# Kernel tuning notes

Measured on AMD Instinct MI355X. Metric: run time of the kernel, lower is better.

## Reference

```python
import jax, jax.numpy as jnp
import numpy as np

N, QLEN, KLEN = 4, 2048, 2048
QDIM = KVDIM = 512
EMBED, HEADS = 1024, 16
HEAD_DIM = EMBED // HEADS


def setup_inputs() -> dict:
    key = jax.random.key(0)
    ks = jax.random.split(key, 7)
    return {
        "queries": jax.random.normal(ks[0], (N, QLEN, QDIM), dtype=jnp.float32),
        "keys": jax.random.normal(ks[1], (1, KLEN, KVDIM), dtype=jnp.float32),
        "values": jax.random.normal(ks[2], (1, KLEN, KVDIM), dtype=jnp.float32),
        "mask": jax.random.randint(ks[3], (N, 1, 1, KLEN), 0, 2, dtype=jnp.int32),
        "Wq": jax.random.normal(ks[4], (QDIM, EMBED), dtype=jnp.float32) * (QDIM ** -0.5),
        "Wk": jax.random.normal(ks[5], (KVDIM, EMBED), dtype=jnp.float32) * (KVDIM ** -0.5),
        "Wv": jax.random.normal(ks[6], (KVDIM, EMBED), dtype=jnp.float32) * (KVDIM ** -0.5),
    }


def reference(queries, keys, values, mask, Wq, Wk, Wv):
    # Projections (Linear, no bias)
    q = (queries @ Wq).reshape(N, QLEN, HEADS, HEAD_DIM)      # [N, Q, H, D]
    k = (keys @ Wk).reshape(KLEN, HEADS, HEAD_DIM)            # [K, H, D] (batch-1, shared)
    v = (values @ Wv).reshape(KLEN, HEADS, HEAD_DIM)          # [K, H, D]

    # energy: [N, H, Q, K]
    energy = jnp.einsum('nqhd,khd->nhqk', q, k)
    energy = jnp.where(mask == 0, jnp.float32(-1e20), energy)
    attn = jax.nn.softmax(energy / jnp.float32(HEAD_DIM ** 0.5), axis=3)

    out = jnp.einsum('nhqk,khd->nqhd', attn, v)               # [N, Q, H, D]
    return out.reshape(N, QLEN, EMBED)
```

## Files before the change

kernel.cpp:

```cpp
#include <hip/hip_runtime.h>

#define NB 4
#define QLEN 2048
#define KLEN 2048
#define QDIM 512
#define EMBED 1024
#define HEADS 16
#define HD 64

typedef __bf16 bf16x8 __attribute__((ext_vector_type(8)));
typedef float f32x2 __attribute__((ext_vector_type(2)));
typedef float f32x4 __attribute__((ext_vector_type(4)));
typedef float f32x16 __attribute__((ext_vector_type(16)));

#define CLOG 0.18033688011112042f

__device__ __forceinline__ float fexp2(float x) {
#if __has_builtin(__builtin_amdgcn_exp2f)
    return __builtin_amdgcn_exp2f(x);
#else
    float r;
    asm("v_exp_f32 %0, %1\n\ts_nop 1" : "=v"(r) : "v"(x));
    return r;
#endif
}

#if __has_builtin(__builtin_amdgcn_sched_barrier)
#define SCHED_FENCE() __builtin_amdgcn_sched_barrier(0)
#else
#define SCHED_FENCE()
#endif

__device__ __forceinline__ void dma16(const void* g, void* l) {
    __builtin_amdgcn_global_load_lds(
        (const __attribute__((address_space(1))) void*)g,
        (__attribute__((address_space(3))) void*)l, 16, 0, 0);
}

__global__ __launch_bounds__(256) void prep(const float* __restrict__ q,
                                            const float* __restrict__ k,
                                            const float* __restrict__ v,
                                            const float* __restrict__ Wq,
                                            const float* __restrict__ Wk,
                                            const float* __restrict__ Wv,
                                            __bf16* __restrict__ qd,
                                            __bf16* __restrict__ kd,
                                            __bf16* __restrict__ vd,
                                            __bf16* __restrict__ WtQ,
                                            __bf16* __restrict__ WtK,
                                            __bf16* __restrict__ WtV) {
    __shared__ float tile[32][33];
    int b = blockIdx.x, tid = threadIdx.x;
    if (b < 3072) {
        const float* src; __bf16* dst; int cb;
        if (b < 2048)      { src = q; dst = qd; cb = b; }
        else if (b < 2560) { src = k; dst = kd; cb = b - 2048; }
        else               { src = v; dst = vd; cb = b - 2560; }
        int i = (cb * 256 + tid) * 8;
        float4 a0 = *(const float4*)&src[i];
        float4 a1 = *(const float4*)&src[i + 4];
        bf16x8 o;
        o[0] = (__bf16)a0.x; o[1] = (__bf16)a0.y; o[2] = (__bf16)a0.z; o[3] = (__bf16)a0.w;
        o[4] = (__bf16)a1.x; o[5] = (__bf16)a1.y; o[6] = (__bf16)a1.z; o[7] = (__bf16)a1.w;
        *(bf16x8*)&dst[i] = o;
    } else {
        int tb = b - 3072;
        int which = tb >> 9, r = tb & 511;
        const float* src = (which == 0) ? Wq : (which == 1) ? Wk : Wv;
        __bf16* dst = (which == 0) ? WtQ : (which == 1) ? WtK : WtV;
        float scale = (which == 0) ? CLOG : 1.0f;
        int e0 = (r & 31) * 32, c0 = (r >> 5) * 32;
        int tx = tid & 31, ty = tid >> 5;
        for (int i = 0; i < 4; i++)
            tile[ty + 8 * i][tx] = src[(c0 + ty + 8 * i) * EMBED + e0 + tx];
        __syncthreads();
        for (int i = 0; i < 4; i++)
            dst[(e0 + ty + 8 * i) * QDIM + c0 + tx] = (__bf16)(tile[tx][ty + 8 * i] * scale);
    }
}

__device__ __forceinline__ void gemm_compute(const __bf16* As, const __bf16* Bs,
                                             int wr, int wc, int r16, int qq,
                                             f32x4 (&acc)[4][4]) {
    bf16x8 af[4], bq[4];
#pragma unroll
    for (int i = 0; i < 4; i++)
        af[i] = *(const bf16x8*)&As[(wr * 64 + i * 16 + r16) * 32 + qq * 8];
#pragma unroll
    for (int j = 0; j < 4; j++)
        bq[j] = *(const bf16x8*)&Bs[(wc * 64 + j * 16 + r16) * 32 + qq * 8];
#pragma unroll
    for (int i = 0; i < 4; i++)
#pragma unroll
        for (int j = 0; j < 4; j++)
            acc[i][j] = __builtin_amdgcn_mfma_f32_16x16x32_bf16(af[i], bq[j], acc[i][j], 0, 0, 0);
}

__device__ __forceinline__ void gemm128(const __bf16* __restrict__ A,
                                        const __bf16* __restrict__ Bt,
                                        __bf16* As0, __bf16* As1,
                                        __bf16* Bs0, __bf16* Bs1,
                                        int row0, int col0, f32x4 (&acc)[4][4]) {
    int tid = threadIdx.x, wave = tid >> 6, lane = tid & 63;
    int r16 = lane & 15, qq = lane >> 4;
    int wr = wave >> 1, wc = wave & 1;
    const __bf16* agp1 = A + (size_t)(row0 + (tid >> 2)) * QDIM + (tid & 3) * 8;
    const __bf16* agp2 = A + (size_t)(row0 + 64 + (tid >> 2)) * QDIM + (tid & 3) * 8;
    const __bf16* bgp1 = Bt + (size_t)(col0 + (tid >> 2)) * QDIM + (tid & 3) * 8;
    const __bf16* bgp2 = Bt + (size_t)(col0 + 64 + (tid >> 2)) * QDIM + (tid & 3) * 8;
    __bf16 *a0a = &As0[wave * 512], *a0b = &As0[2048 + wave * 512];
    __bf16 *a1a = &As1[wave * 512], *a1b = &As1[2048 + wave * 512];
    __bf16 *b0a = &Bs0[wave * 512], *b0b = &Bs0[2048 + wave * 512];
    __bf16 *b1a = &Bs1[wave * 512], *b1b = &Bs1[2048 + wave * 512];

    dma16(agp1, a0a); dma16(agp2, a0b);
    dma16(bgp1, b0a); dma16(bgp2, b0b);
    agp1 += 32; agp2 += 32; bgp1 += 32; bgp2 += 32;
    __syncthreads();

    for (int t = 0; t < 16; t += 2) {
        dma16(agp1, a1a); dma16(agp2, a1b);
        dma16(bgp1, b1a); dma16(bgp2, b1b);
        agp1 += 32; agp2 += 32; bgp1 += 32; bgp2 += 32;
        SCHED_FENCE();
        gemm_compute(As0, Bs0, wr, wc, r16, qq, acc);
        __syncthreads();
        if (t + 2 < 16) {
            dma16(agp1, a0a); dma16(agp2, a0b);
            dma16(bgp1, b0a); dma16(bgp2, b0b);
            agp1 += 32; agp2 += 32; bgp1 += 32; bgp2 += 32;
        }
        SCHED_FENCE();
        gemm_compute(As1, Bs1, wr, wc, r16, qq, acc);
        __syncthreads();
    }
}

__global__ __launch_bounds__(256) void proj_all(const __bf16* __restrict__ qin,
                                                const __bf16* __restrict__ kin,
                                                const __bf16* __restrict__ vin,
                                                const __bf16* __restrict__ wtq,
                                                const __bf16* __restrict__ wtk,
                                                const __bf16* __restrict__ wtv,
                                                __bf16* __restrict__ qout,
                                                __bf16* __restrict__ kout,
                                                __bf16* __restrict__ vtout) {
    __shared__ __align__(16) __bf16 As[2][128 * 32];
    __shared__ __align__(16) __bf16 Bs[2][128 * 32];
    int bid = blockIdx.x;
    const __bf16 *A, *Bt;
    int mode, b;
    if (bid < 512)      { A = qin; Bt = wtq; mode = 0; b = bid; }
    else if (bid < 640) { A = kin; Bt = wtk; mode = 1; b = bid - 512; }
    else                { A = wtv; Bt = vin; mode = 2; b = bid - 640; }
    int row0, col0;
    if (mode == 2) { row0 = (b >> 4) * 128; col0 = (b & 15) * 128; }
    else           { row0 = (b >> 3) * 128; col0 = (b & 7) * 128; }
    f32x4 acc[4][4] = {};
    gemm128(A, Bt, As[0], As[1], Bs[0], Bs[1], row0, col0, acc);
    int lane = threadIdx.x & 63, wave = threadIdx.x >> 6;
    int r16 = lane & 15, qq = lane >> 4;
    int wr = wave >> 1, wc = wave & 1;
#pragma unroll
    for (int i = 0; i < 4; i++)
#pragma unroll
        for (int j = 0; j < 4; j++)
#pragma unroll
            for (int rr = 0; rr < 4; rr++) {
                int grow = row0 + wr * 64 + i * 16 + qq * 4 + rr;
                int gcol = col0 + wc * 64 + j * 16 + r16;
                __bf16 v = (__bf16)acc[i][j][rr];
                if (mode == 0) {
                    int hh = gcol >> 6, d = gcol & 63;
                    int n = grow >> 11, qr = grow & 2047;
                    qout[((size_t)(n * HEADS + hh) * QLEN + qr) * HD + d] = v;
                } else if (mode == 1) {
                    int hh = gcol >> 6, d = gcol & 63;
                    kout[((size_t)hh * KLEN + grow) * HD + d] = v;
                } else {
                    vtout[(size_t)grow * KLEN + gcol] = v;
                }
            }
}

__device__ __forceinline__ void attn_tile(const __bf16* ksb, const __bf16* vsb,
                                          const float* mrow, const bf16x8 (&qfrag)[4],
                                          int col, int h,
                                          f32x16& o0, f32x16& o1, f32x2& rsl) {
    bf16x8 pfrag[4];
#pragma unroll
    for (int kt2 = 0; kt2 < 2; kt2++) {
        int R = kt2 * 32 + col;
        union { f32x16 v; f32x4 q[4]; } su;
#pragma unroll
        for (int G = 0; G < 4; G++)
            su.q[G] = *(const f32x4*)&mrow[kt2 * 32 + 16 * (G >> 1) + 8 * h + 4 * (G & 1)];
        f32x16 s = su.v;
        __builtin_amdgcn_s_setprio(1);
#pragma unroll
        for (int c = 0; c < 4; c++) {
            int cc = (2 * c + h) ^ (R & 7);
            bf16x8 kf = *(const bf16x8*)&ksb[(R * 8 + cc) * 8];
            s = __builtin_amdgcn_mfma_f32_32x32x16_bf16(kf, qfrag[c], s, 0, 0, 0);
        }
        __builtin_amdgcn_s_setprio(0);
#pragma unroll
        for (int G = 0; G < 4; G++) {
            int ci = 2 * kt2 + (G >> 1), e0 = (G & 1) * 4;
#pragma unroll
            for (int rr = 0; rr < 4; rr += 2) {
                float p0 = fexp2(s[4 * G + rr]);
                float p1 = fexp2(s[4 * G + rr + 1]);
                f32x2 pp; pp[0] = p0; pp[1] = p1;
                rsl += pp;
                pfrag[ci][e0 + rr] = (__bf16)p0;
                pfrag[ci][e0 + rr + 1] = (__bf16)p1;
            }
        }
    }
    __builtin_amdgcn_s_setprio(1);
#pragma unroll
    for (int c = 0; c < 4; c++) {
        int cc = (2 * c + h) ^ (col & 7);
        bf16x8 v0 = *(const bf16x8*)&vsb[(col * 8 + cc) * 8];
        bf16x8 v1 = *(const bf16x8*)&vsb[((32 + col) * 8 + cc) * 8];
        o0 = __builtin_amdgcn_mfma_f32_32x32x16_bf16(v0, pfrag[c], o0, 0, 0, 0);
        o1 = __builtin_amdgcn_mfma_f32_32x32x16_bf16(v1, pfrag[c], o1, 0, 0, 0);
    }
    __builtin_amdgcn_s_setprio(0);
}

__global__ __launch_bounds__(512, 4) void attn_kernel(const __bf16* __restrict__ qb,
                                                      const __bf16* __restrict__ kb,
                                                      const __bf16* __restrict__ vtb,
                                                      const int* __restrict__ mask,
                                                      float* __restrict__ out) {
    __shared__ __align__(16) __bf16 ks[2][4096];
    __shared__ __align__(16) __bf16 vs[2][4096];
    __shared__ __align__(16) float msf[KLEN];

    int tid = threadIdx.x, wave = tid >> 6, lane = tid & 63;
    int col = lane & 31, h = lane >> 5;
    int q0 = blockIdx.x * 256, hh = blockIdx.y, n = blockIdx.z;
    const __bf16* qg = qb + ((size_t)(n * HEADS + hh) * QLEN + q0 + wave * 32 + col) * HD;
    const __bf16* kg = kb + (size_t)hh * KLEN * HD;
    const __bf16* vg = vtb + (size_t)hh * HD * KLEN;
    const int* mg = mask + n * KLEN;

    bf16x8 qfrag[4];
#pragma unroll
    for (int c = 0; c < 4; c++) qfrag[c] = *(const bf16x8*)&qg[c * 16 + h * 8];

    int R1 = tid >> 3, c1 = (tid & 7) ^ (R1 & 7);
    int g1 = (R1 & 0x33) | ((R1 & 4) << 1) | ((R1 & 8) >> 1);
    const __bf16* kgp1 = kg + g1 * HD + c1 * 8;
    const __bf16* vgp1 = vg + (size_t)R1 * KLEN + c1 * 8;
    __bf16 *kl0 = &ks[0][wave * 512], *kl1 = &ks[1][wave * 512];
    __bf16 *vl0 = &vs[0][wave * 512], *vl1 = &vs[1][wave * 512];

    dma16(kgp1, kl0); dma16(vgp1, vl0);
    kgp1 += 64 * HD; vgp1 += 64;
    {
        int i4 = tid * 4;
        int4 ma = *(const int4*)&mg[i4];
        f32x4 fa;
        fa[0] = ma.x ? 0.f : -1e30f; fa[1] = ma.y ? 0.f : -1e30f;
        fa[2] = ma.z ? 0.f : -1e30f; fa[3] = ma.w ? 0.f : -1e30f;
        *(f32x4*)&msf[i4] = fa;
    }
    __syncthreads();

    f32x16 o0 = {}, o1 = {};
    f32x2 rsl = {};

    for (int t = 0; t < 32; t += 2) {
        dma16(kgp1, kl1); dma16(vgp1, vl1);
        kgp1 += 64 * HD; vgp1 += 64;
        SCHED_FENCE();
        attn_tile(ks[0], vs[0], &msf[t * 64], qfrag, col, h, o0, o1, rsl);
        __syncthreads();
        if (t + 2 < 32) {
            dma16(kgp1, kl0); dma16(vgp1, vl0);
            kgp1 += 64 * HD; vgp1 += 64;
        }
        SCHED_FENCE();
        attn_tile(ks[1], vs[1], &msf[(t + 1) * 64], qfrag, col, h, o0, o1, rsl);
        __syncthreads();
    }

    float rs = rsl[0] + rsl[1];
    rs += __shfl_xor(rs, 32);
    float inv = 1.0f / rs;
    float* op = out + ((size_t)n * QLEN + q0 + wave * 32 + col) * EMBED + hh * HD;
#pragma unroll
    for (int G = 0; G < 4; G++) {
        float4 t0, t1;
        t0.x = o0[4 * G + 0] * inv; t0.y = o0[4 * G + 1] * inv;
        t0.z = o0[4 * G + 2] * inv; t0.w = o0[4 * G + 3] * inv;
        t1.x = o1[4 * G + 0] * inv; t1.y = o1[4 * G + 1] * inv;
        t1.z = o1[4 * G + 2] * inv; t1.w = o1[4 * G + 3] * inv;
        *(float4*)&op[8 * G + 4 * h] = t0;
        *(float4*)&op[32 + 8 * G + 4 * h] = t1;
    }
}

extern "C" void kernel_launch(void* const* d_in, const int* in_sizes, int n_in,
                              void* d_out, int out_size, void* d_ws, size_t ws_size,
                              hipStream_t stream) {
    const float* queries = (const float*)d_in[0];
    const float* keys    = (const float*)d_in[1];
    const float* values  = (const float*)d_in[2];
    const int*   mask    = (const int*)d_in[3];
    const float* Wq      = (const float*)d_in[4];
    const float* Wk      = (const float*)d_in[5];
    const float* Wv      = (const float*)d_in[6];
    float* out = (float*)d_out;

    const size_t MiB = 1048576;
    char* ws = (char*)d_ws;
    __bf16* qbf   = (__bf16*)(ws);
    __bf16* kbf   = (__bf16*)(ws + 16 * MiB);
    __bf16* vtbf  = (__bf16*)(ws + 20 * MiB);
    __bf16* wtq   = (__bf16*)(ws + 24 * MiB);
    __bf16* wtk   = (__bf16*)(ws + 25 * MiB);
    __bf16* wtv   = (__bf16*)(ws + 26 * MiB);
    __bf16* qin   = (__bf16*)(ws + 27 * MiB);
    __bf16* kin   = (__bf16*)(ws + 35 * MiB);
    __bf16* vin   = (__bf16*)(ws + 37 * MiB);

    prep<<<4608, 256, 0, stream>>>(queries, keys, values, Wq, Wk, Wv,
                                   qin, kin, vin, wtq, wtk, wtv);
    proj_all<<<768, 256, 0, stream>>>(qin, kin, vin, wtq, wtk, wtv, qbf, kbf, vtbf);
    attn_kernel<<<dim3(QLEN / 256, HEADS, NB), 512, 0, stream>>>(qbf, kbf, vtbf, mask, out);
}
```

Before: 181.5 us.

## Compact unmasked keys per batch and skip masked key tiles in attention

Prep now builds a prefix-sum index of unmasked key positions for each batch, and the K/V projection scatters only those rows into per-batch compacted K and V^T buffers, zero-padded to a 64-row tile. The attention kernel loops over only the tiles that hold live keys, drops the additive mask, and subtracts the padding's exp(0) contributions from the row sum. This removes roughly half of the attention work for a random mask, at the cost of per-batch K/V copies (four times the writes), scattered stores in the projection, and a serial scan block in prep. It also changes behaviour when every key is masked (the reference gives a uniform softmax, while here the sum becomes zero).

```diff
diff --git a/kernel.cpp b/kernel.cpp
--- a/kernel.cpp
+++ b/kernel.cpp
@@ -43,15 +43,57 @@
                                             const float* __restrict__ Wq,
                                             const float* __restrict__ Wk,
                                             const float* __restrict__ Wv,
+                                            const int* __restrict__ mask,
                                             __bf16* __restrict__ qd,
                                             __bf16* __restrict__ kd,
                                             __bf16* __restrict__ vd,
                                             __bf16* __restrict__ WtQ,
                                             __bf16* __restrict__ WtK,
-                                            __bf16* __restrict__ WtV) {
+                                            __bf16* __restrict__ WtV,
+                                            int* __restrict__ pidx,
+                                            int* __restrict__ cntg,
+                                            __bf16* __restrict__ kbf,
+                                            __bf16* __restrict__ vtbf) {
     __shared__ float tile[32][33];
+    __shared__ int part[256];
     int b = blockIdx.x, tid = threadIdx.x;
-    if (b < 3072) {
+    if (b >= 4608) {
+        int n = b - 4608;
+        const int* mp = mask + n * KLEN + tid * 8;
+        int4 ma = *(const int4*)&mp[0];
+        int4 mb = *(const int4*)&mp[4];
+        int m[8] = { ma.x, ma.y, ma.z, ma.w, mb.x, mb.y, mb.z, mb.w };
+        int c = 0;
+#pragma unroll
+        for (int j = 0; j < 8; j++) c += (m[j] != 0);
+        part[tid] = c;
+        __syncthreads();
+        for (int off = 1; off < 256; off <<= 1) {
+            int vv = (tid >= off) ? part[tid - off] : 0;
+            __syncthreads();
+            part[tid] += vv;
+            __syncthreads();
+        }
+        int pos = part[tid] - c;
+        int* pw = pidx + n * KLEN + tid * 8;
+#pragma unroll
+        for (int j = 0; j < 8; j++) {
+            pw[j] = m[j] ? pos : -1;
+            pos += (m[j] != 0);
+        }
+        int cnt = part[255];
+        if (tid == 0) cntg[n] = cnt;
+        int tiles = (cnt + 63) >> 6, pe = tiles << 6, np = pe - cnt;
+        for (int h = 0; h < HEADS; h++) {
+            __bf16* kb0 = kbf + (((size_t)(n * HEADS + h)) * KLEN + cnt) * HD;
+            __bf16* vb0 = vtbf + ((size_t)(n * HEADS + h)) * HD * KLEN;
+            for (int i = tid; i < np * HD; i += 256) {
+                int r = i >> 6, d = i & 63;
+                kb0[r * HD + d] = (__bf16)0.f;
+                vb0[(size_t)d * KLEN + cnt + r] = (__bf16)0.f;
+            }
+        }
+    } else if (b < 3072) {
         const float* src; __bf16* dst; int cb;
         if (b < 2048)      { src = q; dst = qd; cb = b; }
         else if (b < 2560) { src = k; dst = kd; cb = b - 2048; }
@@ -142,6 +184,7 @@
                                                 const __bf16* __restrict__ wtq,
                                                 const __bf16* __restrict__ wtk,
                                                 const __bf16* __restrict__ wtv,
+                                                const int* __restrict__ pidx,
                                                 __bf16* __restrict__ qout,
                                                 __bf16* __restrict__ kout,
                                                 __bf16* __restrict__ vtout) {
@@ -176,26 +219,32 @@
                     qout[((size_t)(n * HEADS + hh) * QLEN + qr) * HD + d] = v;
                 } else if (mode == 1) {
                     int hh = gcol >> 6, d = gcol & 63;
-                    kout[((size_t)hh * KLEN + grow) * HD + d] = v;
+#pragma unroll
+                    for (int nn = 0; nn < NB; nn++) {
+                        int p = pidx[nn * KLEN + grow];
+                        if (p >= 0)
+                            kout[((size_t)(nn * HEADS + hh) * KLEN + p) * HD + d] = v;
+                    }
                 } else {
-                    vtout[(size_t)grow * KLEN + gcol] = v;
+#pragma unroll
+                    for (int nn = 0; nn < NB; nn++) {
+                        int p = pidx[nn * KLEN + gcol];
+                        if (p >= 0)
+                            vtout[((size_t)nn * EMBED + grow) * KLEN + p] = v;
+                    }
                 }
             }
 }
 
 __device__ __forceinline__ void attn_tile(const __bf16* ksb, const __bf16* vsb,
-                                          const float* mrow, const bf16x8 (&qfrag)[4],
+                                          const bf16x8 (&qfrag)[4],
                                           int col, int h,
                                           f32x16& o0, f32x16& o1, f32x2& rsl) {
     bf16x8 pfrag[4];
 #pragma unroll
     for (int kt2 = 0; kt2 < 2; kt2++) {
         int R = kt2 * 32 + col;
-        union { f32x16 v; f32x4 q[4]; } su;
-#pragma unroll
-        for (int G = 0; G < 4; G++)
-            su.q[G] = *(const f32x4*)&mrow[kt2 * 32 + 16 * (G >> 1) + 8 * h + 4 * (G & 1)];
-        f32x16 s = su.v;
+        f32x16 s = {};
         __builtin_amdgcn_s_setprio(1);
 #pragma unroll
         for (int c = 0; c < 4; c++) {
@@ -233,19 +282,20 @@
 __global__ __launch_bounds__(512, 4) void attn_kernel(const __bf16* __restrict__ qb,
                                                       const __bf16* __restrict__ kb,
                                                       const __bf16* __restrict__ vtb,
-                                                      const int* __restrict__ mask,
+                                                      const int* __restrict__ cntg,
                                                       float* __restrict__ out) {
     __shared__ __align__(16) __bf16 ks[2][4096];
     __shared__ __align__(16) __bf16 vs[2][4096];
-    __shared__ __align__(16) float msf[KLEN];
 
     int tid = threadIdx.x, wave = tid >> 6, lane = tid & 63;
     int col = lane & 31, h = lane >> 5;
     int q0 = blockIdx.x * 256, hh = blockIdx.y, n = blockIdx.z;
+    int cnt = cntg[n];
+    int tiles = (cnt + 63) >> 6;
+    int npad = (tiles << 6) - cnt;
     const __bf16* qg = qb + ((size_t)(n * HEADS + hh) * QLEN + q0 + wave * 32 + col) * HD;
-    const __bf16* kg = kb + (size_t)hh * KLEN * HD;
-    const __bf16* vg = vtb + (size_t)hh * HD * KLEN;
-    const int* mg = mask + n * KLEN;
+    const __bf16* kg = kb + (size_t)(n * HEADS + hh) * KLEN * HD;
+    const __bf16* vg = vtb + (size_t)(n * HEADS + hh) * HD * KLEN;
 
     bf16x8 qfrag[4];
 #pragma unroll
@@ -255,41 +305,28 @@
     int g1 = (R1 & 0x33) | ((R1 & 4) << 1) | ((R1 & 8) >> 1);
     const __bf16* kgp1 = kg + g1 * HD + c1 * 8;
     const __bf16* vgp1 = vg + (size_t)R1 * KLEN + c1 * 8;
-    __bf16 *kl0 = &ks[0][wave * 512], *kl1 = &ks[1][wave * 512];
-    __bf16 *vl0 = &vs[0][wave * 512], *vl1 = &vs[1][wave * 512];
-
-    dma16(kgp1, kl0); dma16(vgp1, vl0);
+
+    dma16(kgp1, &ks[0][wave * 512]); dma16(vgp1, &vs[0][wave * 512]);
     kgp1 += 64 * HD; vgp1 += 64;
-    {
-        int i4 = tid * 4;
-        int4 ma = *(const int4*)&mg[i4];
-        f32x4 fa;
-        fa[0] = ma.x ? 0.f : -1e30f; fa[1] = ma.y ? 0.f : -1e30f;
-        fa[2] = ma.z ? 0.f : -1e30f; fa[3] = ma.w ? 0.f : -1e30f;
-        *(f32x4*)&msf[i4] = fa;
-    }
     __syncthreads();
 
     f32x16 o0 = {}, o1 = {};
     f32x2 rsl = {};
 
-    for (int t = 0; t < 32; t += 2) {
-        dma16(kgp1, kl1); dma16(vgp1, vl1);
-        kgp1 += 64 * HD; vgp1 += 64;
+    for (int t = 0; t < tiles; t++) {
+        int pc = t & 1, pn = pc ^ 1;
+        if (t + 1 < tiles) {
+            dma16(kgp1, &ks[pn][wave * 512]); dma16(vgp1, &vs[pn][wave * 512]);
+            kgp1 += 64 * HD; vgp1 += 64;
+        }
         SCHED_FENCE();
-        attn_tile(ks[0], vs[0], &msf[t * 64], qfrag, col, h, o0, o1, rsl);
-        __syncthreads();
-        if (t + 2 < 32) {
-            dma16(kgp1, kl0); dma16(vgp1, vl0);
-            kgp1 += 64 * HD; vgp1 += 64;
-        }
-        SCHED_FENCE();
-        attn_tile(ks[1], vs[1], &msf[(t + 1) * 64], qfrag, col, h, o0, o1, rsl);
+        attn_tile(ks[pc], vs[pc], qfrag, col, h, o0, o1, rsl);
         __syncthreads();
     }
 
     float rs = rsl[0] + rsl[1];
     rs += __shfl_xor(rs, 32);
+    rs -= (float)npad;
     float inv = 1.0f / rs;
     float* op = out + ((size_t)n * QLEN + q0 + wave * 32 + col) * EMBED + hh * HD;
 #pragma unroll
@@ -320,16 +357,20 @@
     char* ws = (char*)d_ws;
     __bf16* qbf   = (__bf16*)(ws);
     __bf16* kbf   = (__bf16*)(ws + 16 * MiB);
-    __bf16* vtbf  = (__bf16*)(ws + 20 * MiB);
-    __bf16* wtq   = (__bf16*)(ws + 24 * MiB);
-    __bf16* wtk   = (__bf16*)(ws + 25 * MiB);
-    __bf16* wtv   = (__bf16*)(ws + 26 * MiB);
-    __bf16* qin   = (__bf16*)(ws + 27 * MiB);
-    __bf16* kin   = (__bf16*)(ws + 35 * MiB);
-    __bf16* vin   = (__bf16*)(ws + 37 * MiB);
-
-    prep<<<4608, 256, 0, stream>>>(queries, keys, values, Wq, Wk, Wv,
-                                   qin, kin, vin, wtq, wtk, wtv);
-    proj_all<<<768, 256, 0, stream>>>(qin, kin, vin, wtq, wtk, wtv, qbf, kbf, vtbf);
-    attn_kernel<<<dim3(QLEN / 256, HEADS, NB), 512, 0, stream>>>(qbf, kbf, vtbf, mask, out);
-}
+    __bf16* vtbf  = (__bf16*)(ws + 32 * MiB);
+    __bf16* wtq   = (__bf16*)(ws + 48 * MiB);
+    __bf16* wtk   = (__bf16*)(ws + 49 * MiB);
+    __bf16* wtv   = (__bf16*)(ws + 50 * MiB);
+    __bf16* qin   = (__bf16*)(ws + 51 * MiB);
+    __bf16* kin   = (__bf16*)(ws + 59 * MiB);
+    __bf16* vin   = (__bf16*)(ws + 61 * MiB);
+    int*    pidx  = (int*)(ws + 63 * MiB);
+    int*    cntg  = (int*)(ws + 63 * MiB + 65536);
+
+    prep<<<4612, 256, 0, stream>>>(queries, keys, values, Wq, Wk, Wv, mask,
+                                   qin, kin, vin, wtq, wtk, wtv,
+                                   pidx, cntg, kbf, vtbf);
+    proj_all<<<768, 256, 0, stream>>>(qin, kin, vin, wtq, wtk, wtv, pidx,
+                                      qbf, kbf, vtbf);
+    attn_kernel<<<dim3(QLEN / 256, HEADS, NB), 512, 0, stream>>>(qbf, kbf, vtbf, cntg, out);
+}
```

New measurement: 227.0 us. +25.1%, slower.
